# Optimization experiments

Measured on AMD Instinct MI355X. Metric: run time of the kernel, lower is better.

Reference implementation:

```python
import jax, jax.numpy as jnp
import numpy as np
import math

B, T, D = 4, 4096, 512   # batch, seq, n_embd
E, K, H = 4, 2, 4 * 512  # num_experts, top_experts, expert hidden


def gelu_gpt2(x):
    # 0.5*x*(1+tanh(sqrt(2/pi)*(x+0.044715*x^3)))
    c = math.sqrt(2.0 / math.pi)
    return 0.5 * x * (1.0 + jnp.tanh(c * (x + 0.044715 * x ** 3)))


def setup_inputs() -> dict:
    key = jax.random.key(0)
    ks = jax.random.split(key, 5)
    s = 0.02
    return {
        "x": jax.random.normal(ks[0], (B, T, D), dtype=jnp.float32),
        "gate_w": (jax.random.normal(ks[1], (E, D)) * s).astype(jnp.float32),  # nn.Linear weight [out,in]
        "w1": (jax.random.normal(ks[2], (E, H, D)) * s).astype(jnp.float32),
        "b1": jnp.zeros((E, H), dtype=jnp.float32),
        "w2": (jax.random.normal(ks[3], (E, D, H)) * s).astype(jnp.float32),
        "b2": jnp.zeros((E, D), dtype=jnp.float32),
    }


def reference(x, gate_w, w1, b1, w2, b2):
    d = x.shape[-1]
    xf = x.reshape(-1, d)                              # [N, D]
    gate = xf @ gate_w.T                               # [N, E]
    # load_balancing_loss: torch.mean over dims (0,1) of a 2D tensor -> scalar
    m = jnp.mean(gate)
    balancing_loss = jnp.sum(m * jnp.log(m + 0.1))
    # top-k routing + softmax over selected logits (computed in fp32)
    w, idx = jax.lax.top_k(gate, K)                    # [N, K]
    w = jax.nn.softmax(w.astype(jnp.float32), axis=1).astype(x.dtype)
    # dense combine weights [N, E]; zero for unselected experts -> identical math
    cw = jnp.sum(jax.nn.one_hot(idx, E, dtype=x.dtype) * w[..., None], axis=1)
    # run every expert on every token, weighted combine (dropout = eval identity)
    h = jnp.einsum('nd,ehd->neh', xf, w1) + b1         # [N, E, H]
    h = gelu_gpt2(h)
    o = jnp.einsum('neh,edh->ned', h, w2) + b2         # [N, E, D]
    out = jnp.einsum('ned,ne->nd', o, cw)              # [N, D]
    return out.reshape(x.shape), balancing_loss
```

## Files before the change

### kernel.cpp

```cpp
#include <hip/hip_runtime.h>
#include <hip/hip_bf16.h>
#include <cmath>
#include <cstdint>

#define N_TOK 16384
#define DIM   512
#define HID   2048
#define NEXP  4

typedef __attribute__((ext_vector_type(8))) short bf16x8;
typedef __attribute__((ext_vector_type(4))) float f32x4;

__device__ __forceinline__ short f2bf(float f) {
  __hip_bfloat16 h = __float2bfloat16(f);
  return *reinterpret_cast<short*>(&h);
}

__device__ __forceinline__ float gelu_f(float v) {
  const float c = 0.7978845608028654f;
  return 0.5f * v * (1.0f + tanhf(c * (v + 0.044715f * v * v * v)));
}

__device__ __forceinline__ void load_lds16(const void* g, void* l) {
  __builtin_amdgcn_global_load_lds(
      (const __attribute__((address_space(1))) void*)g,
      (__attribute__((address_space(3))) void*)l, 16, 0, 0);
}

__global__ void cvt_kernel(const float* __restrict__ src, short* __restrict__ dst, int n4) {
  int i = blockIdx.x * blockDim.x + threadIdx.x;
  int stride = gridDim.x * blockDim.x;
  for (; i < n4; i += stride) {
    float4 v = reinterpret_cast<const float4*>(src)[i];
    short4 o;
    o.x = f2bf(v.x); o.y = f2bf(v.y); o.z = f2bf(v.z); o.w = f2bf(v.w);
    reinterpret_cast<short4*>(dst)[i] = o;
  }
}

__global__ __launch_bounds__(256) void gate_kernel(
    const float* __restrict__ x, const float* __restrict__ gw,
    float* __restrict__ cw, float* __restrict__ gate_sum,
    short* __restrict__ xb) {
  int t = threadIdx.x, wid = t >> 6, lane = t & 63;

  float4 g[NEXP][2];
#pragma unroll
  for (int e = 0; e < NEXP; ++e) {
    const float4* gp = reinterpret_cast<const float4*>(gw + e * DIM + lane * 8);
    g[e][0] = gp[0]; g[e][1] = gp[1];
  }

  float lsum = 0.0f;
  int n0 = blockIdx.x * 64 + wid * 16;
  for (int i = 0; i < 16; ++i) {
    int n = n0 + i;
    const float4* xr4 = reinterpret_cast<const float4*>(x + (size_t)n * DIM);
    float4 a = xr4[lane * 2];
    float4 b = xr4[lane * 2 + 1];

    short4 s0, s1;
    s0.x = f2bf(a.x); s0.y = f2bf(a.y); s0.z = f2bf(a.z); s0.w = f2bf(a.w);
    s1.x = f2bf(b.x); s1.y = f2bf(b.y); s1.z = f2bf(b.z); s1.w = f2bf(b.w);
    short4* xbp = reinterpret_cast<short4*>(xb + (size_t)n * DIM + lane * 8);
    xbp[0] = s0; xbp[1] = s1;

    float p[NEXP];
#pragma unroll
    for (int e = 0; e < NEXP; ++e) {
      p[e] = a.x * g[e][0].x + a.y * g[e][0].y + a.z * g[e][0].z + a.w * g[e][0].w
           + b.x * g[e][1].x + b.y * g[e][1].y + b.z * g[e][1].z + b.w * g[e][1].w;
    }
#pragma unroll
    for (int e = 0; e < NEXP; ++e)
#pragma unroll
      for (int off = 32; off; off >>= 1) p[e] += __shfl_xor(p[e], off);

    if (lane == 0) {
      lsum += p[0] + p[1] + p[2] + p[3];
      int i0 = 0;
#pragma unroll
      for (int e = 1; e < NEXP; ++e) if (p[e] > p[i0]) i0 = e;
      int i1 = -1;
#pragma unroll
      for (int e = 0; e < NEXP; ++e) {
        if (e == i0) continue;
        if (i1 < 0 || p[e] > p[i1]) i1 = e;
      }
      float eb = expf(p[i1] - p[i0]);
      float w0 = 1.0f / (1.0f + eb);
      float w1 = eb / (1.0f + eb);
      float row[NEXP] = {0.f, 0.f, 0.f, 0.f};
      row[i0] = w0; row[i1] = w1;
#pragma unroll
      for (int e = 0; e < NEXP; ++e) cw[n * NEXP + e] = row[e];
    }
  }
  __shared__ float bs[4];
  if (lane == 0) bs[wid] = lsum;
  __syncthreads();
  if (t == 0) atomicAdd(gate_sum, bs[0] + bs[1] + bs[2] + bs[3]);
}

__global__ void loss_kernel(const float* __restrict__ gate_sum, float* __restrict__ out_loss) {
  float m = gate_sum[0] / (float)(N_TOK * NEXP);
  out_loss[0] = m * logf(m + 0.1f);
}

__global__ __launch_bounds__(256) void count_kernel(const float* __restrict__ cw,
                                                    int* __restrict__ blockcnt) {
  __shared__ int c[4];
  int t = threadIdx.x;
  if (t < 4) c[t] = 0;
  __syncthreads();
  int n = blockIdx.x * 256 + t;
  float4 w = reinterpret_cast<const float4*>(cw)[n];
  unsigned long long m0 = __ballot(w.x != 0.f);
  unsigned long long m1 = __ballot(w.y != 0.f);
  unsigned long long m2 = __ballot(w.z != 0.f);
  unsigned long long m3 = __ballot(w.w != 0.f);
  if ((t & 63) == 0) {
    atomicAdd(&c[0], (int)__popcll(m0));
    atomicAdd(&c[1], (int)__popcll(m1));
    atomicAdd(&c[2], (int)__popcll(m2));
    atomicAdd(&c[3], (int)__popcll(m3));
  }
  __syncthreads();
  if (t < 4) blockcnt[blockIdx.x * 4 + t] = c[t];
}

__global__ void scan_kernel(const int* __restrict__ blockcnt, int* __restrict__ blockoff,
                            int* __restrict__ counts, int* __restrict__ expbase) {
  int lane = threadIdx.x;
  int tot[NEXP];
#pragma unroll
  for (int e = 0; e < NEXP; ++e) {
    int v = blockcnt[lane * 4 + e];
    int inc = v;
#pragma unroll
    for (int off = 1; off < 64; off <<= 1) {
      int u = __shfl_up(inc, off);
      if (lane >= off) inc += u;
    }
    blockoff[lane * 4 + e] = inc - v;
    tot[e] = __shfl(inc, 63);
  }
  if (lane == 0) {
    int base = 0;
#pragma unroll
    for (int e = 0; e < NEXP; ++e) {
      counts[e] = tot[e];
      expbase[e] = base;
      base += tot[e];
    }
  }
}

__global__ __launch_bounds__(256) void write_kernel(const float* __restrict__ cw,
                                                    const int* __restrict__ blockoff,
                                                    const int* __restrict__ expbase,
                                                    int* __restrict__ list) {
  int t = threadIdx.x, wave = t >> 6, lane = t & 63;
  int blk = blockIdx.x;
  int n = blk * 256 + t;
  float4 w4 = reinterpret_cast<const float4*>(cw)[n];
  float wf[4] = {w4.x, w4.y, w4.z, w4.w};
  __shared__ int wcnt[4][4];
  unsigned long long lt = (1ULL << lane) - 1ULL;
  int pfx[4]; bool sel[4];
#pragma unroll
  for (int e = 0; e < NEXP; ++e) {
    sel[e] = (wf[e] != 0.f);
    unsigned long long m = __ballot(sel[e]);
    pfx[e] = (int)__popcll(m & lt);
    if (lane == 0) wcnt[wave][e] = (int)__popcll(m);
  }
  __syncthreads();
#pragma unroll
  for (int e = 0; e < NEXP; ++e) {
    if (sel[e]) {
      int woff = 0;
      for (int w2 = 0; w2 < wave; ++w2) woff += wcnt[w2][e];
      list[expbase[e] + blockoff[blk * 4 + e] + woff + pfx[e]] = n;
    }
  }
}

__global__ __launch_bounds__(256) void moe_gemm1(
    const short* __restrict__ xb, const short* __restrict__ w1b,
    const float* __restrict__ b1, short* __restrict__ Hc,
    const int* __restrict__ list, const int* __restrict__ counts,
    const int* __restrict__ expbase) {
  int e = blockIdx.z;
  int cnt = counts[e];
  int bm0 = blockIdx.y * 128;
  if (bm0 >= cnt) return;
  int base = expbase[e];
  int bn0 = blockIdx.x * 128;
  const short* Bw = w1b + (size_t)e * HID * DIM;

  int t = threadIdx.x, lane = t & 63, wid = t >> 6;
  int srow = t >> 3, scol = (t & 7) * 8;
  const short* Ag[4];
#pragma unroll
  for (int i = 0; i < 4; ++i) {
    int rc = bm0 + i * 32 + srow;
    int tok = list[base + ((rc < cnt) ? rc : 0)];
    Ag[i] = xb + (size_t)tok * DIM + scol;
  }
  const short* Bg = Bw + (size_t)(bn0 + srow) * DIM + scol;

  __shared__ __align__(16) short As[128 * 64];
  __shared__ __align__(16) short Bs[128 * 64];
  f32x4 acc[4][4] = {};
  int wr = (wid >> 1) * 64, wc = (wid & 1) * 64;

  for (int kt = 0; kt < DIM / 64; ++kt) {
    if (kt) __syncthreads();
    int k0 = kt * 64;
#pragma unroll
    for (int i = 0; i < 4; ++i) {
      load_lds16(Ag[i] + k0, As + i * 2048 + t * 8);
      load_lds16(Bg + (size_t)(i * 32) * DIM + k0, Bs + i * 2048 + t * 8);
    }
    __syncthreads();
#pragma unroll
    for (int ks = 0; ks < 2; ++ks) {
      int koff = ks * 32 + ((lane >> 4) << 3);
      bf16x8 af[4], bfr[4];
#pragma unroll
      for (int mi = 0; mi < 4; ++mi)
        af[mi] = *(const bf16x8*)&As[(wr + mi * 16 + (lane & 15)) * 64 + koff];
#pragma unroll
      for (int ni = 0; ni < 4; ++ni)
        bfr[ni] = *(const bf16x8*)&Bs[(wc + ni * 16 + (lane & 15)) * 64 + koff];
#pragma unroll
      for (int mi = 0; mi < 4; ++mi)
#pragma unroll
        for (int ni = 0; ni < 4; ++ni)
          acc[mi][ni] = __builtin_amdgcn_mfma_f32_16x16x32_bf16(af[mi], bfr[ni], acc[mi][ni], 0, 0, 0);
    }
  }

  int crow = (lane >> 4) * 4, ccol = lane & 15;
#pragma unroll
  for (int mi = 0; mi < 4; ++mi) {
#pragma unroll
    for (int ni = 0; ni < 4; ++ni) {
      int col = bn0 + wc + ni * 16 + ccol;
      float bv = b1[(size_t)e * HID + col];
#pragma unroll
      for (int j = 0; j < 4; ++j) {
        int rc = bm0 + wr + mi * 16 + crow + j;
        if (rc < cnt)
          Hc[(size_t)(base + rc) * HID + col] = f2bf(gelu_f(acc[mi][ni][j] + bv));
      }
    }
  }
}

__global__ __launch_bounds__(256) void moe_gemm2(
    const short* __restrict__ Hc, const short* __restrict__ w2b,
    const float* __restrict__ b2, float* __restrict__ out,
    const float* __restrict__ cw, const int* __restrict__ list,
    const int* __restrict__ counts, const int* __restrict__ expbase) {
  int e = blockIdx.z;
  int cnt = counts[e];
  int bm0 = blockIdx.y * 128;
  if (bm0 >= cnt) return;
  int base = expbase[e];
  int bn0 = blockIdx.x * 128;
  const short* Bw = w2b + (size_t)e * DIM * HID;

  int t = threadIdx.x, lane = t & 63, wid = t >> 6;
  int srow = t >> 3, scol = (t & 7) * 8;
  const short* Ag = Hc + (size_t)(base + bm0 + srow) * HID + scol;
  const short* Bg = Bw + (size_t)(bn0 + srow) * HID + scol;

  __shared__ __align__(16) short As[128 * 64];
  __shared__ __align__(16) short Bs[128 * 64];
  f32x4 acc[4][4] = {};
  int wr = (wid >> 1) * 64, wc = (wid & 1) * 64;

  for (int kt = 0; kt < HID / 64; ++kt) {
    if (kt) __syncthreads();
    int k0 = kt * 64;
#pragma unroll
    for (int i = 0; i < 4; ++i) {
      load_lds16(Ag + (size_t)(i * 32) * HID + k0, As + i * 2048 + t * 8);
      load_lds16(Bg + (size_t)(i * 32) * HID + k0, Bs + i * 2048 + t * 8);
    }
    __syncthreads();
#pragma unroll
    for (int ks = 0; ks < 2; ++ks) {
      int koff = ks * 32 + ((lane >> 4) << 3);
      bf16x8 af[4], bfr[4];
#pragma unroll
      for (int mi = 0; mi < 4; ++mi)
        af[mi] = *(const bf16x8*)&As[(wr + mi * 16 + (lane & 15)) * 64 + koff];
#pragma unroll
      for (int ni = 0; ni < 4; ++ni)
        bfr[ni] = *(const bf16x8*)&Bs[(wc + ni * 16 + (lane & 15)) * 64 + koff];
#pragma unroll
      for (int mi = 0; mi < 4; ++mi)
#pragma unroll
        for (int ni = 0; ni < 4; ++ni)
          acc[mi][ni] = __builtin_amdgcn_mfma_f32_16x16x32_bf16(af[mi], bfr[ni], acc[mi][ni], 0, 0, 0);
    }
  }

  int crow = (lane >> 4) * 4, ccol = lane & 15;
#pragma unroll
  for (int mi = 0; mi < 4; ++mi) {
#pragma unroll
    for (int ni = 0; ni < 4; ++ni) {
      int col = bn0 + wc + ni * 16 + ccol;
      float bv = b2[(size_t)e * DIM + col];
#pragma unroll
      for (int j = 0; j < 4; ++j) {
        int rc = bm0 + wr + mi * 16 + crow + j;
        if (rc < cnt) {
          int tok = list[base + rc];
          float wgt = cw[tok * NEXP + e];
          atomicAdd(&out[(size_t)tok * DIM + col], wgt * (acc[mi][ni][j] + bv));
        }
      }
    }
  }
}

template <int KDIM, int EPI>
__global__ __launch_bounds__(256) void gemm_kernel(
    const short* __restrict__ A, const short* __restrict__ B,
    const float* __restrict__ bias,
    short* __restrict__ Hout, float* __restrict__ out,
    const float* __restrict__ cw, int expert) {
  constexpr int BK = 64;
  __shared__ __align__(16) short As[128 * BK];
  __shared__ __align__(16) short Bs[128 * BK];
  int t = threadIdx.x;
  int lane = t & 63, wid = t >> 6;
  int bn0 = blockIdx.x * 128;
  int bm0 = blockIdx.y * 128;
  int wr = (wid >> 1) * 64;
  int wc = (wid & 1) * 64;
  f32x4 acc[4][4] = {};
  int srow = t >> 3;
  int scol = (t & 7) * 8;
  const short* Ag = A + (size_t)(bm0 + srow) * KDIM + scol;
  const short* Bg = B + (size_t)(bn0 + srow) * KDIM + scol;
  for (int kt = 0; kt < KDIM / BK; ++kt) {
    if (kt) __syncthreads();
    int k0 = kt * BK;
#pragma unroll
    for (int i = 0; i < 4; ++i) {
      load_lds16(Ag + (size_t)(i * 32) * KDIM + k0, As + i * 2048 + t * 8);
      load_lds16(Bg + (size_t)(i * 32) * KDIM + k0, Bs + i * 2048 + t * 8);
    }
    __syncthreads();
#pragma unroll
    for (int ks = 0; ks < 2; ++ks) {
      int koff = ks * 32 + ((lane >> 4) << 3);
      bf16x8 af[4], bfr[4];
#pragma unroll
      for (int mi = 0; mi < 4; ++mi)
        af[mi] = *(const bf16x8*)&As[(wr + mi * 16 + (lane & 15)) * BK + koff];
#pragma unroll
      for (int ni = 0; ni < 4; ++ni)
        bfr[ni] = *(const bf16x8*)&Bs[(wc + ni * 16 + (lane & 15)) * BK + koff];
#pragma unroll
      for (int mi = 0; mi < 4; ++mi)
#pragma unroll
        for (int ni = 0; ni < 4; ++ni)
          acc[mi][ni] = __builtin_amdgcn_mfma_f32_16x16x32_bf16(af[mi], bfr[ni], acc[mi][ni], 0, 0, 0);
    }
  }
  int crow = (lane >> 4) * 4;
  int ccol = lane & 15;
#pragma unroll
  for (int mi = 0; mi < 4; ++mi) {
#pragma unroll
    for (int ni = 0; ni < 4; ++ni) {
      int col = bn0 + wc + ni * 16 + ccol;
      float bv = bias[col];
#pragma unroll
      for (int j = 0; j < 4; ++j) {
        int row = bm0 + wr + mi * 16 + crow + j;
        float v = acc[mi][ni][j] + bv;
        if constexpr (EPI == 0) {
          Hout[(size_t)row * HID + col] = f2bf(gelu_f(v));
        } else {
          float w = cw[row * NEXP + expert];
          float r = w * v;
          if constexpr (EPI == 1) out[(size_t)row * DIM + col] = r;
          else                    out[(size_t)row * DIM + col] += r;
        }
      }
    }
  }
}

extern "C" void kernel_launch(void* const* d_in, const int* in_sizes, int n_in,
                              void* d_out, int out_size, void* d_ws, size_t ws_size,
                              hipStream_t stream) {
  const float* x  = (const float*)d_in[0];
  const float* gw = (const float*)d_in[1];
  const float* w1 = (const float*)d_in[2];
  const float* b1 = (const float*)d_in[3];
  const float* w2 = (const float*)d_in[4];
  const float* b2 = (const float*)d_in[5];
  float* out = (float*)d_out;

  char* ws = (char*)d_ws;
  float* cw       = (float*)(ws + 0);
  float* gate_sum = (float*)(ws + 262144);
  int*   blockcnt = (int*)(ws + 262400);
  int*   blockoff = (int*)(ws + 263424);
  int*   counts   = (int*)(ws + 264448);
  int*   expbase  = (int*)(ws + 264704);
  int*   list     = (int*)(ws + 264960);
  short* xb       = (short*)(ws + 396032);
  short* w1b      = (short*)(ws + 17173248);
  short* w2b      = (short*)(ws + 25561856);
  short* Hc       = (short*)(ws + 33950464);
  const size_t ROUTED_NEED = 33950464ull + (size_t)(32768 + 128) * HID * 2;

  hipMemsetAsync(gate_sum, 0, sizeof(float), stream);
  cvt_kernel<<<1024, 256, 0, stream>>>(w1, w1b, NEXP * HID * DIM / 4);
  cvt_kernel<<<1024, 256, 0, stream>>>(w2, w2b, NEXP * DIM * HID / 4);
  gate_kernel<<<N_TOK / 64, 256, 0, stream>>>(x, gw, cw, gate_sum, xb);
  loss_kernel<<<1, 1, 0, stream>>>(gate_sum, out + (size_t)N_TOK * DIM);

  if (ws_size >= ROUTED_NEED) {
    hipMemsetAsync(out, 0, (size_t)N_TOK * DIM * sizeof(float), stream);
    count_kernel<<<64, 256, 0, stream>>>(cw, blockcnt);
    scan_kernel<<<1, 64, 0, stream>>>(blockcnt, blockoff, counts, expbase);
    write_kernel<<<64, 256, 0, stream>>>(cw, blockoff, expbase, list);
    moe_gemm1<<<dim3(HID / 128, N_TOK / 128, NEXP), 256, 0, stream>>>(
        xb, w1b, b1, Hc, list, counts, expbase);
    moe_gemm2<<<dim3(DIM / 128, N_TOK / 128, NEXP), 256, 0, stream>>>(
        Hc, w2b, b2, out, cw, list, counts, expbase);
  } else {
    short* Hb = (short*)(ws + 33816832);
    for (int e = 0; e < NEXP; ++e) {
      gemm_kernel<DIM, 0><<<dim3(HID / 128, N_TOK / 128), 256, 0, stream>>>(
          xb, w1b + (size_t)e * HID * DIM, b1 + (size_t)e * HID, Hb, nullptr, nullptr, e);
      if (e == 0)
        gemm_kernel<HID, 1><<<dim3(DIM / 128, N_TOK / 128), 256, 0, stream>>>(
            Hb, w2b + (size_t)e * DIM * HID, b2 + (size_t)e * DIM, nullptr, out, cw, e);
      else
        gemm_kernel<HID, 2><<<dim3(DIM / 128, N_TOK / 128), 256, 0, stream>>>(
            Hb, w2b + (size_t)e * DIM * HID, b2 + (size_t)e * DIM, nullptr, out, cw, e);
    }
  }
}
```

Before: 498.7 us.

## Swizzle LDS tiles and serialize per-expert GEMM2 to replace atomics

```diff
diff --git a/kernel.cpp b/kernel.cpp
--- a/kernel.cpp
+++ b/kernel.cpp
@@ -26,6 +26,8 @@
       (const __attribute__((address_space(1))) void*)g,
       (__attribute__((address_space(3))) void*)l, 16, 0, 0);
 }
+
+#define LDSIDX(r, c16) (((r) * 64) + ((((c16) ^ ((r) & 7)) * 8)))
 
 __global__ void cvt_kernel(const float* __restrict__ src, short* __restrict__ dst, int n4) {
   int i = blockIdx.x * blockDim.x + threadIdx.x;
@@ -200,7 +202,8 @@
   const short* Bw = w1b + (size_t)e * HID * DIM;
 
   int t = threadIdx.x, lane = t & 63, wid = t >> 6;
-  int srow = t >> 3, scol = (t & 7) * 8;
+  int srow = t >> 3;
+  int scol = ((t & 7) ^ (srow & 7)) * 8;
   const short* Ag[4];
 #pragma unroll
   for (int i = 0; i < 4; ++i) {
@@ -226,14 +229,17 @@
     __syncthreads();
 #pragma unroll
     for (int ks = 0; ks < 2; ++ks) {
-      int koff = ks * 32 + ((lane >> 4) << 3);
       bf16x8 af[4], bfr[4];
 #pragma unroll
-      for (int mi = 0; mi < 4; ++mi)
-        af[mi] = *(const bf16x8*)&As[(wr + mi * 16 + (lane & 15)) * 64 + koff];
-#pragma unroll
-      for (int ni = 0; ni < 4; ++ni)
-        bfr[ni] = *(const bf16x8*)&Bs[(wc + ni * 16 + (lane & 15)) * 64 + koff];
+      for (int mi = 0; mi < 4; ++mi) {
+        int r = wr + mi * 16 + (lane & 15);
+        af[mi] = *(const bf16x8*)&As[LDSIDX(r, ks * 4 + (lane >> 4))];
+      }
+#pragma unroll
+      for (int ni = 0; ni < 4; ++ni) {
+        int r = wc + ni * 16 + (lane & 15);
+        bfr[ni] = *(const bf16x8*)&Bs[LDSIDX(r, ks * 4 + (lane >> 4))];
+      }
 #pragma unroll
       for (int mi = 0; mi < 4; ++mi)
 #pragma unroll
@@ -263,8 +269,8 @@
     const short* __restrict__ Hc, const short* __restrict__ w2b,
     const float* __restrict__ b2, float* __restrict__ out,
     const float* __restrict__ cw, const int* __restrict__ list,
-    const int* __restrict__ counts, const int* __restrict__ expbase) {
-  int e = blockIdx.z;
+    const int* __restrict__ counts, const int* __restrict__ expbase,
+    int e) {
   int cnt = counts[e];
   int bm0 = blockIdx.y * 128;
   if (bm0 >= cnt) return;
@@ -273,7 +279,8 @@
   const short* Bw = w2b + (size_t)e * DIM * HID;
 
   int t = threadIdx.x, lane = t & 63, wid = t >> 6;
-  int srow = t >> 3, scol = (t & 7) * 8;
+  int srow = t >> 3;
+  int scol = ((t & 7) ^ (srow & 7)) * 8;
   const short* Ag = Hc + (size_t)(base + bm0 + srow) * HID + scol;
   const short* Bg = Bw + (size_t)(bn0 + srow) * HID + scol;
 
@@ -293,14 +300,17 @@
     __syncthreads();
 #pragma unroll
     for (int ks = 0; ks < 2; ++ks) {
-      int koff = ks * 32 + ((lane >> 4) << 3);
       bf16x8 af[4], bfr[4];
 #pragma unroll
-      for (int mi = 0; mi < 4; ++mi)
-        af[mi] = *(const bf16x8*)&As[(wr + mi * 16 + (lane & 15)) * 64 + koff];
-#pragma unroll
-      for (int ni = 0; ni < 4; ++ni)
-        bfr[ni] = *(const bf16x8*)&Bs[(wc + ni * 16 + (lane & 15)) * 64 + koff];
+      for (int mi = 0; mi < 4; ++mi) {
+        int r = wr + mi * 16 + (lane & 15);
+        af[mi] = *(const bf16x8*)&As[LDSIDX(r, ks * 4 + (lane >> 4))];
+      }
+#pragma unroll
+      for (int ni = 0; ni < 4; ++ni) {
+        int r = wc + ni * 16 + (lane & 15);
+        bfr[ni] = *(const bf16x8*)&Bs[LDSIDX(r, ks * 4 + (lane >> 4))];
+      }
 #pragma unroll
       for (int mi = 0; mi < 4; ++mi)
 #pragma unroll
@@ -312,18 +322,23 @@
   int crow = (lane >> 4) * 4, ccol = lane & 15;
 #pragma unroll
   for (int mi = 0; mi < 4; ++mi) {
+    int tokr[4]; float wgtr[4]; bool val[4];
+#pragma unroll
+    for (int j = 0; j < 4; ++j) {
+      int rc = bm0 + wr + mi * 16 + crow + j;
+      val[j] = (rc < cnt);
+      int tok = list[base + (val[j] ? rc : 0)];
+      tokr[j] = tok;
+      wgtr[j] = cw[tok * NEXP + e];
+    }
 #pragma unroll
     for (int ni = 0; ni < 4; ++ni) {
       int col = bn0 + wc + ni * 16 + ccol;
       float bv = b2[(size_t)e * DIM + col];
 #pragma unroll
       for (int j = 0; j < 4; ++j) {
-        int rc = bm0 + wr + mi * 16 + crow + j;
-        if (rc < cnt) {
-          int tok = list[base + rc];
-          float wgt = cw[tok * NEXP + e];
-          atomicAdd(&out[(size_t)tok * DIM + col], wgt * (acc[mi][ni][j] + bv));
-        }
+        if (val[j])
+          out[(size_t)tokr[j] * DIM + col] += wgtr[j] * (acc[mi][ni][j] + bv);
       }
     }
   }
@@ -438,8 +453,9 @@
     write_kernel<<<64, 256, 0, stream>>>(cw, blockoff, expbase, list);
     moe_gemm1<<<dim3(HID / 128, N_TOK / 128, NEXP), 256, 0, stream>>>(
         xb, w1b, b1, Hc, list, counts, expbase);
-    moe_gemm2<<<dim3(DIM / 128, N_TOK / 128, NEXP), 256, 0, stream>>>(
-        Hc, w2b, b2, out, cw, list, counts, expbase);
+    for (int e = 0; e < NEXP; ++e)
+      moe_gemm2<<<dim3(DIM / 128, N_TOK / 128), 256, 0, stream>>>(
+          Hc, w2b, b2, out, cw, list, counts, expbase, e);
   } else {
     short* Hb = (short*)(ws + 33816832);
     for (int e = 0; e < NEXP; ++e) {
```

Result: slower. 512.2 us (+2.7%).
